# Kernel tuning notes

Measured on AMD Instinct MI355X. Metric: run time of the kernel, lower is better.

Reference implementation:

```python
import jax, jax.numpy as jnp
import numpy as np

K = 512      # num_embeddings
D = 64       # embedding_dim
N, H, W = 64, 64, 64


def setup_inputs() -> dict:
    key = jax.random.key(0)
    k1, k2 = jax.random.split(key)
    z_e = jax.random.normal(k1, (N, D, H, W), dtype=jnp.float32)
    # torch init: uniform_(-1/K, 1/K)
    emb_weight = jax.random.uniform(k2, (K, D), dtype=jnp.float32,
                                    minval=-1.0 / K, maxval=1.0 / K)
    return {"z_e": z_e, "emb_weight": emb_weight}


def reference(z_e, emb_weight):
    n, d, h, w = z_e.shape
    # (N, D, H, W) -> (N*H*W, D)
    z_flat = jnp.transpose(z_e, (0, 2, 3, 1)).reshape(-1, d)
    # squared L2 distances via ||z||^2 + ||e||^2 - 2 z.e
    z_sq = jnp.sum(z_flat * z_flat, axis=1, keepdims=True)        # (M, 1)
    e_sq = jnp.sum(emb_weight * emb_weight, axis=1)               # (K,)
    dots = z_flat @ emb_weight.T                                  # (M, K)
    distances = z_sq + e_sq - 2.0 * dots
    indices = jnp.argmin(distances, axis=1)                       # (M,)
    z_q_flat = emb_weight[indices]                                # gather (M, D)
    # vq loss: mse(stop_grad(z_e), z_q)
    diff = jax.lax.stop_gradient(z_flat) - z_q_flat
    vq_loss = jnp.mean(diff * diff)
    # straight-through estimator
    z_q_st = z_flat + jax.lax.stop_gradient(z_q_flat - z_flat)
    z_q = jnp.transpose(z_q_st.reshape(n, h, w, d), (0, 3, 1, 2))
    return z_q, vq_loss, indices.reshape(n, h, w)
```

## Files before the change

kernel.cpp:

```cpp
#include <hip/hip_runtime.h>

#define VQ_D   64
#define VQ_K   512
#define VQ_HW  4096
#define VQ_M   262144
#define VQ_LOSS_OFF 16777216
#define VQ_IDX_OFF  16777217

#define VQ_EPS  1e-4f

typedef float  f32x4  __attribute__((ext_vector_type(4)));
typedef short  bf16x8 __attribute__((ext_vector_type(8)));

__device__ __forceinline__ unsigned short f2bf_rne(float f) {
    unsigned u = __float_as_uint(f);
    u += 0x7FFFu + ((u >> 16) & 1u);
    return (unsigned short)(u >> 16);
}
__device__ __forceinline__ float bf2f(unsigned short h) {
    return __uint_as_float(((unsigned)h) << 16);
}
__device__ __forceinline__ int ldx(int slot) {
    return (slot << 4) ^ (((slot >> 4) & 3) << 4);
}

__global__ void vq_prep(const float* __restrict__ emb, float* __restrict__ esq) {
#pragma clang fp contract(off)
    int k = blockIdx.x * 256 + threadIdx.x;
    if (k < VQ_K) {
        const float* e = emb + k * VQ_D;
        float p[VQ_D];
#pragma unroll
        for (int d = 0; d < VQ_D; ++d) p[d] = e[d] * e[d];
        float r[8];
#pragma unroll
        for (int j = 0; j < 8; ++j) r[j] = p[j];
#pragma unroll
        for (int i = 8; i < VQ_D; i += 8)
#pragma unroll
            for (int j = 0; j < 8; ++j) r[j] += p[i + j];
        esq[k] = ((r[0] + r[1]) + (r[2] + r[3])) + ((r[4] + r[5]) + (r[6] + r[7]));
    }
}

__global__ __launch_bounds__(256, 4) void vq_main(
        const float* __restrict__ z_e,
        const float* __restrict__ emb,
        const float* __restrict__ esq,
        float* __restrict__ out)
{
#pragma clang fp contract(off)
    __shared__ __align__(16) char lbh[16384];
    __shared__ __align__(16) char lbl[16384];
    __shared__ float lesq[512];

    const int tid  = threadIdx.x;
    const int wave = tid >> 6, lane = tid & 63;
    const int c15  = lane & 15, g = lane >> 4;

    lesq[tid]       = esq[tid];
    lesq[tid + 256] = esq[tid + 256];

    const int mblk = blockIdx.x * 128;
    const int n    = mblk >> 12;
    const int hwb  = (mblk & 4095) + wave * 32;
    const float* zn = z_e + (size_t)n * 262144;

    bf16x8 ah[2][2], al[2][2];
#pragma unroll
    for (int ms = 0; ms < 2; ++ms) {
        const int hw = hwb + ms * 16 + c15;
#pragma unroll
        for (int s = 0; s < 2; ++s) {
#pragma unroll
            for (int e = 0; e < 8; ++e) {
                const int d = 32 * s + 8 * g + e;
                float f = zn[(size_t)d * 4096 + hw];
                unsigned short h = f2bf_rne(f);
                ah[ms][s][e] = (short)h;
                al[ms][s][e] = (short)f2bf_rne(f - bf2f(h));
            }
        }
    }

    float best[2][4], sec[2][4];
    int   bidx[2][4];
#pragma unroll
    for (int ms = 0; ms < 2; ++ms)
#pragma unroll
        for (int r = 0; r < 4; ++r) {
            best[ms][r] = 3.4e38f; sec[ms][r] = 3.4e38f; bidx[ms][r] = 0;
        }

    for (int ph = 0; ph < 4; ++ph) {
        __syncthreads();
#pragma unroll
        for (int j = 0; j < 4; ++j) {
            const int f8  = j * 256 + tid;
            const int row = f8 >> 3;
            const int ch  = f8 & 7;
            const float* src = emb + ((ph * 128 + row) * 64 + ch * 8);
            float x[8];
            *(f32x4*)&x[0] = *(const f32x4*)(src);
            *(f32x4*)&x[4] = *(const f32x4*)(src + 4);
            bf16x8 vh, vl;
#pragma unroll
            for (int e = 0; e < 8; ++e) {
                unsigned short h = f2bf_rne(x[e]);
                vh[e] = (short)h;
                vl[e] = (short)f2bf_rne(x[e] - bf2f(h));
            }
            const int s  = ch >> 2, gg = ch & 3;
            const int tl = row >> 4, cc = row & 15;
            const int slot = (tl * 2 + s) * 64 + gg * 16 + cc;
            *(bf16x8*)(lbh + ldx(slot)) = vh;
            *(bf16x8*)(lbl + ldx(slot)) = vl;
        }
        __syncthreads();

        bf16x8 cbh0 = *(const bf16x8*)(lbh + ldx(0 * 64 + lane));
        bf16x8 cbh1 = *(const bf16x8*)(lbh + ldx(1 * 64 + lane));
        bf16x8 cbl0 = *(const bf16x8*)(lbl + ldx(0 * 64 + lane));
        bf16x8 cbl1 = *(const bf16x8*)(lbl + ldx(1 * 64 + lane));
#pragma unroll
        for (int tl = 0; tl < 8; ++tl) {
            bf16x8 nbh0, nbh1, nbl0, nbl1;
            if (tl < 7) {
                nbh0 = *(const bf16x8*)(lbh + ldx((tl * 2 + 2) * 64 + lane));
                nbh1 = *(const bf16x8*)(lbh + ldx((tl * 2 + 3) * 64 + lane));
                nbl0 = *(const bf16x8*)(lbl + ldx((tl * 2 + 2) * 64 + lane));
                nbl1 = *(const bf16x8*)(lbl + ldx((tl * 2 + 3) * 64 + lane));
            }
            f32x4 acc0 = {0.f, 0.f, 0.f, 0.f};
            f32x4 acc1 = {0.f, 0.f, 0.f, 0.f};
            acc0 = __builtin_amdgcn_mfma_f32_16x16x32_bf16(ah[0][0], cbh0, acc0, 0, 0, 0);
            acc1 = __builtin_amdgcn_mfma_f32_16x16x32_bf16(ah[1][0], cbh0, acc1, 0, 0, 0);
            acc0 = __builtin_amdgcn_mfma_f32_16x16x32_bf16(ah[0][1], cbh1, acc0, 0, 0, 0);
            acc1 = __builtin_amdgcn_mfma_f32_16x16x32_bf16(ah[1][1], cbh1, acc1, 0, 0, 0);
            acc0 = __builtin_amdgcn_mfma_f32_16x16x32_bf16(al[0][0], cbh0, acc0, 0, 0, 0);
            acc1 = __builtin_amdgcn_mfma_f32_16x16x32_bf16(al[1][0], cbh0, acc1, 0, 0, 0);
            acc0 = __builtin_amdgcn_mfma_f32_16x16x32_bf16(al[0][1], cbh1, acc0, 0, 0, 0);
            acc1 = __builtin_amdgcn_mfma_f32_16x16x32_bf16(al[1][1], cbh1, acc1, 0, 0, 0);
            acc0 = __builtin_amdgcn_mfma_f32_16x16x32_bf16(ah[0][0], cbl0, acc0, 0, 0, 0);
            acc1 = __builtin_amdgcn_mfma_f32_16x16x32_bf16(ah[1][0], cbl0, acc1, 0, 0, 0);
            acc0 = __builtin_amdgcn_mfma_f32_16x16x32_bf16(ah[0][1], cbl1, acc0, 0, 0, 0);
            acc1 = __builtin_amdgcn_mfma_f32_16x16x32_bf16(ah[1][1], cbl1, acc1, 0, 0, 0);

            const int tg = ph * 8 + tl;
            const float ev = lesq[tg * 16 + c15];
            const int   k  = tg * 16 + c15;
#pragma unroll
            for (int r = 0; r < 4; ++r) {
                float v0 = __builtin_fmaf(-2.f, acc0[r], ev);
                bool lt0 = v0 < best[0][r];
                sec[0][r]  = lt0 ? best[0][r] : fminf(sec[0][r], v0);
                best[0][r] = lt0 ? v0 : best[0][r];
                bidx[0][r] = lt0 ? k : bidx[0][r];
                float v1 = __builtin_fmaf(-2.f, acc1[r], ev);
                bool lt1 = v1 < best[1][r];
                sec[1][r]  = lt1 ? best[1][r] : fminf(sec[1][r], v1);
                best[1][r] = lt1 ? v1 : best[1][r];
                bidx[1][r] = lt1 ? k : bidx[1][r];
            }
            cbh0 = nbh0; cbh1 = nbh1; cbl0 = nbl0; cbl1 = nbl1;
        }
    }

#pragma unroll
    for (int ms = 0; ms < 2; ++ms)
#pragma unroll
        for (int r = 0; r < 4; ++r) {
            float b = best[ms][r], s2 = sec[ms][r]; int bi = bidx[ms][r];
#pragma unroll
            for (int off = 1; off <= 8; off <<= 1) {
                float ob = __shfl_xor(b,  off, 64);
                float os = __shfl_xor(s2, off, 64);
                int   oi = __shfl_xor(bi, off, 64);
                bool lt = ob < b;
                float loser = lt ? b : ob;
                s2 = fminf(fminf(s2, os), loser);
                b  = lt ? ob : b;
                bi = lt ? oi : bi;
            }
            best[ms][r] = b; sec[ms][r] = s2; bidx[ms][r] = bi;
        }

    const int srcl = 16 * ((lane & 15) >> 2);
    float bb_ = 3.4e38f, ss_ = 3.4e38f; int ii_ = 0;
#pragma unroll
    for (int ms = 0; ms < 2; ++ms)
#pragma unroll
        for (int r = 0; r < 4; ++r) {
            float gb = __shfl(best[ms][r], srcl, 64);
            float gs = __shfl(sec[ms][r],  srcl, 64);
            int   gi = __shfl(bidx[ms][r], srcl, 64);
            bool hit = (ms == (lane >> 4)) && (r == (lane & 3));
            bb_ = hit ? gb : bb_; ss_ = hit ? gs : ss_; ii_ = hit ? gi : ii_;
        }
    const bool own = lane < 32;

    unsigned long long msk = __ballot(own && (ss_ - bb_ < VQ_EPS));
    while (msk) {
        const int j = __ffsll(msk) - 1;
        msk &= msk - 1;
        const float* zr = zn + hwb + j;
        float r8[8];
#pragma unroll
        for (int dj = 0; dj < 8; ++dj) {
            float f = zr[(size_t)dj * 4096];
            r8[dj] = f * f;
        }
#pragma unroll
        for (int i = 8; i < 64; i += 8)
#pragma unroll
            for (int dj = 0; dj < 8; ++dj) {
                float f = zr[(size_t)(i + dj) * 4096];
                r8[dj] += f * f;
            }
        const float zsq = ((r8[0] + r8[1]) + (r8[2] + r8[3]))
                        + ((r8[4] + r8[5]) + (r8[6] + r8[7]));
        float a[8];
#pragma unroll
        for (int q = 0; q < 8; ++q) a[q] = 0.f;
        const float* er0 = emb + (size_t)(lane * 8) * VQ_D;
        for (int c4 = 0; c4 < 16; ++c4) {
            f32x4 z4;
#pragma unroll
            for (int x = 0; x < 4; ++x) z4[x] = zr[(size_t)(c4 * 4 + x) * 4096];
#pragma unroll
            for (int q = 0; q < 8; ++q) {
                f32x4 e4 = *(const f32x4*)(er0 + q * VQ_D + c4 * 4);
#pragma unroll
                for (int x = 0; x < 4; ++x)
                    a[q] = __builtin_fmaf(z4[x], e4[x], a[q]);
            }
        }
        float fb = 3.4e38f; int fk = 0;
#pragma unroll
        for (int q = 0; q < 8; ++q) {
            const int kk = lane * 8 + q;
            float tt = zsq + lesq[kk];
            float dd = tt - 2.0f * a[q];
            if (dd < fb) { fb = dd; fk = kk; }
        }
#pragma unroll
        for (int off = 32; off > 0; off >>= 1) {
            float ob = __shfl_xor(fb, off, 64);
            int   ok = __shfl_xor(fk, off, 64);
            if (ob < fb || (ob == fb && ok < fk)) { fb = ob; fk = ok; }
        }
        if (lane == j) ii_ = fk;
    }

    if (own)
        out[VQ_IDX_OFF + mblk + wave * 32 + lane] = (float)ii_;
}

__global__ __launch_bounds__(256, 8) void vq_epi(
        const float* __restrict__ z_e,
        const float* __restrict__ emb,
        float* __restrict__ out,
        double* __restrict__ loss_acc)
{
#pragma clang fp contract(off)
    __shared__ float wsum[4];
    const int tid  = threadIdx.x;
    const int wave = tid >> 6, lane = tid & 63;
    const int m    = blockIdx.x * 256 + tid;
    const int n    = m >> 12;
    const int hw   = m & 4095;

    const float* zp = z_e + (size_t)n * 262144 + hw;
    const int ii = (int)out[VQ_IDX_OFF + m];
    const float* eb = emb + (size_t)ii * VQ_D;
    float* op = out + (size_t)n * 262144 + hw;

    float lsum = 0.f;
#pragma unroll
    for (int c4 = 0; c4 < 16; ++c4) {
        f32x4 e4 = *(const f32x4*)(eb + c4 * 4);
#pragma unroll
        for (int x = 0; x < 4; ++x) {
            const int d = c4 * 4 + x;
            float q = e4[x];
            op[(size_t)d * 4096] = q;
            float diff = zp[(size_t)d * 4096] - q;
            lsum = __builtin_fmaf(diff, diff, lsum);
        }
    }

    for (int off = 32; off > 0; off >>= 1)
        lsum += __shfl_down(lsum, off, 64);
    if (lane == 0) wsum[wave] = lsum;
    __syncthreads();
    if (tid == 0) {
        float b = wsum[0] + wsum[1] + wsum[2] + wsum[3];
        atomicAdd(loss_acc, (double)b);
    }
}

__global__ void vq_fin(const double* __restrict__ loss_acc, float* __restrict__ out) {
    if (threadIdx.x == 0)
        out[VQ_LOSS_OFF] = (float)(*loss_acc / 16777216.0);
}

extern "C" void kernel_launch(void* const* d_in, const int* in_sizes, int n_in,
                              void* d_out, int out_size, void* d_ws, size_t ws_size,
                              hipStream_t stream) {
    const float* z_e = (const float*)d_in[0];
    const float* emb = (const float*)d_in[1];
    float* out = (float*)d_out;

    double* loss_acc = (double*)d_ws;
    float*  esq      = (float*)((char*)d_ws + 8);

    (void)hipMemsetAsync(d_ws, 0, 8, stream);
    vq_prep<<<2, 256, 0, stream>>>(emb, esq);
    vq_main<<<VQ_M / 128, 256, 0, stream>>>(z_e, emb, esq, out);
    vq_epi<<<VQ_M / 256, 256, 0, stream>>>(z_e, emb, out, loss_acc);
    vq_fin<<<1, 64, 0, stream>>>(loss_acc, out);
}
```

Before: 309.8 us.

## Halve codebook LDS tiles and defer ambiguous rows to separate rescue kernel

The main kernel now stages 64 codebook rows per phase instead of 128, cutting LDS from about 34KB to 18KB so occupancy can rise (launch bounds 8 instead of 4). Rows whose best and second-best distances are too close are no longer rechecked inline with exact fp32; they are appended to a global list through an atomic and handled by a new grid-stride rescue kernel. This removes divergent serial fp32 work from the hot kernel, at the cost of an extra launch, global atomics, and twice as many barrier phases. A fallback path keeps the old kernel when the workspace is too small.

```diff
diff --git a/kernel.cpp b/kernel.cpp
--- a/kernel.cpp
+++ b/kernel.cpp
@@ -9,6 +9,11 @@
 
 #define VQ_EPS  1e-4f
 
+#define WS_CNT_OFF  8
+#define WS_ESQ_OFF  12
+#define WS_LIST_OFF 2060
+#define WS_NEED     (2060 + 4 * VQ_M)
+
 typedef float  f32x4  __attribute__((ext_vector_type(4)));
 typedef short  bf16x8 __attribute__((ext_vector_type(8)));
 
@@ -43,15 +48,71 @@
     }
 }
 
-__global__ __launch_bounds__(256, 4) void vq_main(
+__device__ __forceinline__ int vq_exact_point(
+        const float* __restrict__ zr,
+        const float* __restrict__ emb,
+        const float* __restrict__ esq,
+        int lane)
+{
+    float r8[8];
+#pragma unroll
+    for (int dj = 0; dj < 8; ++dj) {
+        float f = zr[(size_t)dj * 4096];
+        r8[dj] = f * f;
+    }
+#pragma unroll
+    for (int i = 8; i < 64; i += 8)
+#pragma unroll
+        for (int dj = 0; dj < 8; ++dj) {
+            float f = zr[(size_t)(i + dj) * 4096];
+            r8[dj] += f * f;
+        }
+    const float zsq = ((r8[0] + r8[1]) + (r8[2] + r8[3]))
+                    + ((r8[4] + r8[5]) + (r8[6] + r8[7]));
+    float a[8];
+#pragma unroll
+    for (int q = 0; q < 8; ++q) a[q] = 0.f;
+    const float* er0 = emb + (size_t)(lane * 8) * VQ_D;
+    for (int c4 = 0; c4 < 16; ++c4) {
+        f32x4 z4;
+#pragma unroll
+        for (int x = 0; x < 4; ++x) z4[x] = zr[(size_t)(c4 * 4 + x) * 4096];
+#pragma unroll
+        for (int q = 0; q < 8; ++q) {
+            f32x4 e4 = *(const f32x4*)(er0 + q * VQ_D + c4 * 4);
+#pragma unroll
+            for (int x = 0; x < 4; ++x)
+                a[q] = __builtin_fmaf(z4[x], e4[x], a[q]);
+        }
+    }
+    float fb = 3.4e38f; int fk = 0;
+#pragma unroll
+    for (int q = 0; q < 8; ++q) {
+        const int kk = lane * 8 + q;
+        float tt = zsq + esq[kk];
+        float dd = tt - 2.0f * a[q];
+        if (dd < fb) { fb = dd; fk = kk; }
+    }
+#pragma unroll
+    for (int off = 32; off > 0; off >>= 1) {
+        float ob = __shfl_xor(fb, off, 64);
+        int   ok = __shfl_xor(fk, off, 64);
+        if (ob < fb || (ob == fb && ok < fk)) { fb = ob; fk = ok; }
+    }
+    return fk;
+}
+
+__global__ __launch_bounds__(256, 8) void vq_main_fast(
         const float* __restrict__ z_e,
         const float* __restrict__ emb,
         const float* __restrict__ esq,
-        float* __restrict__ out)
+        float* __restrict__ out,
+        int* __restrict__ cnt_p,
+        int* __restrict__ list)
 {
 #pragma clang fp contract(off)
-    __shared__ __align__(16) char lbh[16384];
-    __shared__ __align__(16) char lbl[16384];
+    __shared__ __align__(16) char lbh[8192];
+    __shared__ __align__(16) char lbl[8192];
     __shared__ float lesq[512];
 
     const int tid  = threadIdx.x;
@@ -92,14 +153,14 @@
             best[ms][r] = 3.4e38f; sec[ms][r] = 3.4e38f; bidx[ms][r] = 0;
         }
 
-    for (int ph = 0; ph < 4; ++ph) {
+    for (int ph = 0; ph < 8; ++ph) {
         __syncthreads();
 #pragma unroll
-        for (int j = 0; j < 4; ++j) {
+        for (int j = 0; j < 2; ++j) {
             const int f8  = j * 256 + tid;
             const int row = f8 >> 3;
             const int ch  = f8 & 7;
-            const float* src = emb + ((ph * 128 + row) * 64 + ch * 8);
+            const float* src = emb + ((ph * 64 + row) * 64 + ch * 8);
             float x[8];
             *(f32x4*)&x[0] = *(const f32x4*)(src);
             *(f32x4*)&x[4] = *(const f32x4*)(src + 4);
@@ -123,9 +184,9 @@
         bf16x8 cbl0 = *(const bf16x8*)(lbl + ldx(0 * 64 + lane));
         bf16x8 cbl1 = *(const bf16x8*)(lbl + ldx(1 * 64 + lane));
 #pragma unroll
-        for (int tl = 0; tl < 8; ++tl) {
-            bf16x8 nbh0, nbh1, nbl0, nbl1;
-            if (tl < 7) {
+        for (int tl = 0; tl < 4; ++tl) {
+            bf16x8 nbh0 = cbh0, nbh1 = cbh1, nbl0 = cbl0, nbl1 = cbl1;
+            if (tl < 3) {
                 nbh0 = *(const bf16x8*)(lbh + ldx((tl * 2 + 2) * 64 + lane));
                 nbh1 = *(const bf16x8*)(lbh + ldx((tl * 2 + 3) * 64 + lane));
                 nbl0 = *(const bf16x8*)(lbl + ldx((tl * 2 + 2) * 64 + lane));
@@ -146,7 +207,7 @@
             acc0 = __builtin_amdgcn_mfma_f32_16x16x32_bf16(ah[0][1], cbl1, acc0, 0, 0, 0);
             acc1 = __builtin_amdgcn_mfma_f32_16x16x32_bf16(ah[1][1], cbl1, acc1, 0, 0, 0);
 
-            const int tg = ph * 8 + tl;
+            const int tg = ph * 4 + tl;
             const float ev = lesq[tg * 16 + c15];
             const int   k  = tg * 16 + c15;
 #pragma unroll
@@ -199,56 +260,206 @@
         }
     const bool own = lane < 32;
 
+    const int m_own = mblk + wave * 32 + lane;
+    unsigned long long amb = __ballot(own && (ss_ - bb_ < VQ_EPS));
+    const int nw = __popcll(amb);
+    int base = 0;
+    if (nw) {
+        if (lane == 0) base = atomicAdd(cnt_p, nw);
+        base = __shfl(base, 0, 64);
+        if (own && (amb >> lane) & 1ull) {
+            const int pos = __popcll(amb & ((1ull << lane) - 1ull));
+            list[base + pos] = m_own;
+        }
+    }
+
+    if (own)
+        out[VQ_IDX_OFF + m_own] = (float)ii_;
+}
+
+__global__ __launch_bounds__(256, 8) void vq_rescue(
+        const float* __restrict__ z_e,
+        const float* __restrict__ emb,
+        const float* __restrict__ esq,
+        float* __restrict__ out,
+        const int* __restrict__ cnt_p,
+        const int* __restrict__ list)
+{
+#pragma clang fp contract(off)
+    const int wave = threadIdx.x >> 6, lane = threadIdx.x & 63;
+    const int gw = blockIdx.x * 4 + wave;
+    const int nw = gridDim.x * 4;
+    const int cnt = *cnt_p;
+    for (int i = gw; i < cnt; i += nw) {
+        const int m = list[i];
+        const int n = m >> 12, hw = m & 4095;
+        const float* zr = z_e + (size_t)n * 262144 + hw;
+        const int fk = vq_exact_point(zr, emb, esq, lane);
+        if (lane == 0) out[VQ_IDX_OFF + m] = (float)fk;
+    }
+}
+
+__global__ __launch_bounds__(256, 4) void vq_main_fb(
+        const float* __restrict__ z_e,
+        const float* __restrict__ emb,
+        const float* __restrict__ esq,
+        float* __restrict__ out)
+{
+#pragma clang fp contract(off)
+    __shared__ __align__(16) char lbh[16384];
+    __shared__ __align__(16) char lbl[16384];
+    __shared__ float lesq[512];
+
+    const int tid  = threadIdx.x;
+    const int wave = tid >> 6, lane = tid & 63;
+    const int c15  = lane & 15, g = lane >> 4;
+
+    lesq[tid]       = esq[tid];
+    lesq[tid + 256] = esq[tid + 256];
+
+    const int mblk = blockIdx.x * 128;
+    const int n    = mblk >> 12;
+    const int hwb  = (mblk & 4095) + wave * 32;
+    const float* zn = z_e + (size_t)n * 262144;
+
+    bf16x8 ah[2][2], al[2][2];
+#pragma unroll
+    for (int ms = 0; ms < 2; ++ms) {
+        const int hw = hwb + ms * 16 + c15;
+#pragma unroll
+        for (int s = 0; s < 2; ++s) {
+#pragma unroll
+            for (int e = 0; e < 8; ++e) {
+                const int d = 32 * s + 8 * g + e;
+                float f = zn[(size_t)d * 4096 + hw];
+                unsigned short h = f2bf_rne(f);
+                ah[ms][s][e] = (short)h;
+                al[ms][s][e] = (short)f2bf_rne(f - bf2f(h));
+            }
+        }
+    }
+
+    float best[2][4], sec[2][4];
+    int   bidx[2][4];
+#pragma unroll
+    for (int ms = 0; ms < 2; ++ms)
+#pragma unroll
+        for (int r = 0; r < 4; ++r) {
+            best[ms][r] = 3.4e38f; sec[ms][r] = 3.4e38f; bidx[ms][r] = 0;
+        }
+
+    for (int ph = 0; ph < 4; ++ph) {
+        __syncthreads();
+#pragma unroll
+        for (int j = 0; j < 4; ++j) {
+            const int f8  = j * 256 + tid;
+            const int row = f8 >> 3;
+            const int ch  = f8 & 7;
+            const float* src = emb + ((ph * 128 + row) * 64 + ch * 8);
+            float x[8];
+            *(f32x4*)&x[0] = *(const f32x4*)(src);
+            *(f32x4*)&x[4] = *(const f32x4*)(src + 4);
+            bf16x8 vh, vl;
+#pragma unroll
+            for (int e = 0; e < 8; ++e) {
+                unsigned short h = f2bf_rne(x[e]);
+                vh[e] = (short)h;
+                vl[e] = (short)f2bf_rne(x[e] - bf2f(h));
+            }
+            const int s  = ch >> 2, gg = ch & 3;
+            const int tl = row >> 4, cc = row & 15;
+            const int slot = (tl * 2 + s) * 64 + gg * 16 + cc;
+            *(bf16x8*)(lbh + ldx(slot)) = vh;
+            *(bf16x8*)(lbl + ldx(slot)) = vl;
+        }
+        __syncthreads();
+
+        bf16x8 cbh0 = *(const bf16x8*)(lbh + ldx(0 * 64 + lane));
+        bf16x8 cbh1 = *(const bf16x8*)(lbh + ldx(1 * 64 + lane));
+        bf16x8 cbl0 = *(const bf16x8*)(lbl + ldx(0 * 64 + lane));
+        bf16x8 cbl1 = *(const bf16x8*)(lbl + ldx(1 * 64 + lane));
+#pragma unroll
+        for (int tl = 0; tl < 8; ++tl) {
+            bf16x8 nbh0 = cbh0, nbh1 = cbh1, nbl0 = cbl0, nbl1 = cbl1;
+            if (tl < 7) {
+                nbh0 = *(const bf16x8*)(lbh + ldx((tl * 2 + 2) * 64 + lane));
+                nbh1 = *(const bf16x8*)(lbh + ldx((tl * 2 + 3) * 64 + lane));
+                nbl0 = *(const bf16x8*)(lbl + ldx((tl * 2 + 2) * 64 + lane));
+                nbl1 = *(const bf16x8*)(lbl + ldx((tl * 2 + 3) * 64 + lane));
+            }
+            f32x4 acc0 = {0.f, 0.f, 0.f, 0.f};
+            f32x4 acc1 = {0.f, 0.f, 0.f, 0.f};
+            acc0 = __builtin_amdgcn_mfma_f32_16x16x32_bf16(ah[0][0], cbh0, acc0, 0, 0, 0);
+            acc1 = __builtin_amdgcn_mfma_f32_16x16x32_bf16(ah[1][0], cbh0, acc1, 0, 0, 0);
+            acc0 = __builtin_amdgcn_mfma_f32_16x16x32_bf16(ah[0][1], cbh1, acc0, 0, 0, 0);
+            acc1 = __builtin_amdgcn_mfma_f32_16x16x32_bf16(ah[1][1], cbh1, acc1, 0, 0, 0);
+            acc0 = __builtin_amdgcn_mfma_f32_16x16x32_bf16(al[0][0], cbh0, acc0, 0, 0, 0);
+            acc1 = __builtin_amdgcn_mfma_f32_16x16x32_bf16(al[1][0], cbh0, acc1, 0, 0, 0);
+            acc0 = __builtin_amdgcn_mfma_f32_16x16x32_bf16(al[0][1], cbh1, acc0, 0, 0, 0);
+            acc1 = __builtin_amdgcn_mfma_f32_16x16x32_bf16(al[1][1], cbh1, acc1, 0, 0, 0);
+            acc0 = __builtin_amdgcn_mfma_f32_16x16x32_bf16(ah[0][0], cbl0, acc0, 0, 0, 0);
+            acc1 = __builtin_amdgcn_mfma_f32_16x16x32_bf16(ah[1][0], cbl0, acc1, 0, 0, 0);
+            acc0 = __builtin_amdgcn_mfma_f32_16x16x32_bf16(ah[0][1], cbl1, acc0, 0, 0, 0);
+            acc1 = __builtin_amdgcn_mfma_f32_16x16x32_bf16(ah[1][1], cbl1, acc1, 0, 0, 0);
+
+            const int tg = ph * 8 + tl;
+            const float ev = lesq[tg * 16 + c15];
+            const int   k  = tg * 16 + c15;
+#pragma unroll
+            for (int r = 0; r < 4; ++r) {
+                float v0 = __builtin_fmaf(-2.f, acc0[r], ev);
+                bool lt0 = v0 < best[0][r];
+                sec[0][r]  = lt0 ? best[0][r] : fminf(sec[0][r], v0);
+                best[0][r] = lt0 ? v0 : best[0][r];
+                bidx[0][r] = lt0 ? k : bidx[0][r];
+                float v1 = __builtin_fmaf(-2.f, acc1[r], ev);
+                bool lt1 = v1 < best[1][r];
+                sec[1][r]  = lt1 ? best[1][r] : fminf(sec[1][r], v1);
+                best[1][r] = lt1 ? v1 : best[1][r];
+                bidx[1][r] = lt1 ? k : bidx[1][r];
+            }
+            cbh0 = nbh0; cbh1 = nbh1; cbl0 = nbl0; cbl1 = nbl1;
+        }
+    }
+
+#pragma unroll
+    for (int ms = 0; ms < 2; ++ms)
+#pragma unroll
+        for (int r = 0; r < 4; ++r) {
+            float b = best[ms][r], s2 = sec[ms][r]; int bi = bidx[ms][r];
+#pragma unroll
+            for (int off = 1; off <= 8; off <<= 1) {
+                float ob = __shfl_xor(b,  off, 64);
+                float os = __shfl_xor(s2, off, 64);
+                int   oi = __shfl_xor(bi, off, 64);
+                bool lt = ob < b;
+                float loser = lt ? b : ob;
+                s2 = fminf(fminf(s2, os), loser);
+                b  = lt ? ob : b;
+                bi = lt ? oi : bi;
+            }
+            best[ms][r] = b; sec[ms][r] = s2; bidx[ms][r] = bi;
+        }
+
+    const int srcl = 16 * ((lane & 15) >> 2);
+    float bb_ = 3.4e38f, ss_ = 3.4e38f; int ii_ = 0;
+#pragma unroll
+    for (int ms = 0; ms < 2; ++ms)
+#pragma unroll
+        for (int r = 0; r < 4; ++r) {
+            float gb = __shfl(best[ms][r], srcl, 64);
+            float gs = __shfl(sec[ms][r],  srcl, 64);
+            int   gi = __shfl(bidx[ms][r], srcl, 64);
+            bool hit = (ms == (lane >> 4)) && (r == (lane & 3));
+            bb_ = hit ? gb : bb_; ss_ = hit ? gs : ss_; ii_ = hit ? gi : ii_;
+        }
+    const bool own = lane < 32;
+
     unsigned long long msk = __ballot(own && (ss_ - bb_ < VQ_EPS));
     while (msk) {
         const int j = __ffsll(msk) - 1;
         msk &= msk - 1;
-        const float* zr = zn + hwb + j;
-        float r8[8];
-#pragma unroll
-        for (int dj = 0; dj < 8; ++dj) {
-            float f = zr[(size_t)dj * 4096];
-            r8[dj] = f * f;
-        }
-#pragma unroll
-        for (int i = 8; i < 64; i += 8)
-#pragma unroll
-            for (int dj = 0; dj < 8; ++dj) {
-                float f = zr[(size_t)(i + dj) * 4096];
-                r8[dj] += f * f;
-            }
-        const float zsq = ((r8[0] + r8[1]) + (r8[2] + r8[3]))
-                        + ((r8[4] + r8[5]) + (r8[6] + r8[7]));
-        float a[8];
-#pragma unroll
-        for (int q = 0; q < 8; ++q) a[q] = 0.f;
-        const float* er0 = emb + (size_t)(lane * 8) * VQ_D;
-        for (int c4 = 0; c4 < 16; ++c4) {
-            f32x4 z4;
-#pragma unroll
-            for (int x = 0; x < 4; ++x) z4[x] = zr[(size_t)(c4 * 4 + x) * 4096];
-#pragma unroll
-            for (int q = 0; q < 8; ++q) {
-                f32x4 e4 = *(const f32x4*)(er0 + q * VQ_D + c4 * 4);
-#pragma unroll
-                for (int x = 0; x < 4; ++x)
-                    a[q] = __builtin_fmaf(z4[x], e4[x], a[q]);
-            }
-        }
-        float fb = 3.4e38f; int fk = 0;
-#pragma unroll
-        for (int q = 0; q < 8; ++q) {
-            const int kk = lane * 8 + q;
-            float tt = zsq + lesq[kk];
-            float dd = tt - 2.0f * a[q];
-            if (dd < fb) { fb = dd; fk = kk; }
-        }
-#pragma unroll
-        for (int off = 32; off > 0; off >>= 1) {
-            float ob = __shfl_xor(fb, off, 64);
-            int   ok = __shfl_xor(fk, off, 64);
-            if (ob < fb || (ob == fb && ok < fk)) { fb = ob; fk = ok; }
-        }
+        const int fk = vq_exact_point(zn + hwb + j, emb, lesq, lane);
         if (lane == j) ii_ = fk;
     }
 
@@ -310,13 +521,26 @@
     const float* z_e = (const float*)d_in[0];
     const float* emb = (const float*)d_in[1];
     float* out = (float*)d_out;
-
-    double* loss_acc = (double*)d_ws;
-    float*  esq      = (float*)((char*)d_ws + 8);
-
-    (void)hipMemsetAsync(d_ws, 0, 8, stream);
-    vq_prep<<<2, 256, 0, stream>>>(emb, esq);
-    vq_main<<<VQ_M / 128, 256, 0, stream>>>(z_e, emb, esq, out);
-    vq_epi<<<VQ_M / 256, 256, 0, stream>>>(z_e, emb, out, loss_acc);
-    vq_fin<<<1, 64, 0, stream>>>(loss_acc, out);
-}
+    char* wsb = (char*)d_ws;
+
+    double* loss_acc = (double*)wsb;
+
+    if (ws_size >= (size_t)WS_NEED) {
+        float* esq = (float*)(wsb + WS_ESQ_OFF);
+        int*   cnt = (int*)(wsb + WS_CNT_OFF);
+        int*   lst = (int*)(wsb + WS_LIST_OFF);
+        (void)hipMemsetAsync(d_ws, 0, 12, stream);
+        vq_prep<<<2, 256, 0, stream>>>(emb, esq);
+        vq_main_fast<<<VQ_M / 128, 256, 0, stream>>>(z_e, emb, esq, out, cnt, lst);
+        vq_rescue<<<256, 256, 0, stream>>>(z_e, emb, esq, out, cnt, lst);
+        vq_epi<<<VQ_M / 256, 256, 0, stream>>>(z_e, emb, out, loss_acc);
+        vq_fin<<<1, 64, 0, stream>>>(loss_acc, out);
+    } else {
+        float* esq = (float*)(wsb + 8);
+        (void)hipMemsetAsync(d_ws, 0, 8, stream);
+        vq_prep<<<2, 256, 0, stream>>>(emb, esq);
+        vq_main_fb<<<VQ_M / 128, 256, 0, stream>>>(z_e, emb, esq, out);
+        vq_epi<<<VQ_M / 256, 256, 0, stream>>>(z_e, emb, out, loss_acc);
+        vq_fin<<<1, 64, 0, stream>>>(loss_acc, out);
+    }
+}
```

Measured after the change: 1.068 ms. 245% more time.
